# Optimization experiments

Measured on AMD Instinct MI355X. Metric: run time of the kernel, lower is better.

## Reference

```python
import jax, jax.numpy as jnp
import numpy as np

TOP_K = 2  # matches init_kwargs top_k


def setup_inputs() -> dict:
    key = jax.random.key(0)
    ks = jax.random.split(key, 7)
    d_model, d_ff, E = 512, 2048, 8
    B, S = 2, 2048
    std = 0.02
    return {
        "x": jax.random.normal(ks[0], (B, S, d_model), dtype=jnp.float32),
        "Wr": jax.random.normal(ks[1], (E, d_model), dtype=jnp.float32) * std,
        "br": jnp.zeros((E,), dtype=jnp.float32),
        "W1": jax.random.normal(ks[2], (E, d_model, d_ff), dtype=jnp.float32) * (1.0 / np.sqrt(d_model)),
        "b1": jnp.zeros((E, d_ff), dtype=jnp.float32),
        "W2": jax.random.normal(ks[3], (E, d_ff, d_model), dtype=jnp.float32) * (1.0 / np.sqrt(d_ff)),
        "b2": jnp.zeros((E, d_model), dtype=jnp.float32),
    }


def _moe_forward(x, Wr, br, W1, b1, W2, b2):
    leading = x.shape[:-1]
    d = x.shape[-1]
    E = Wr.shape[0]
    xf = x.reshape(-1, d)                                   # [N, d]
    N = xf.shape[0]

    # --- token router (linear head) ---
    logits = xf @ Wr.T + br                                  # [N, E]
    routing = jax.nn.softmax(logits, axis=-1)                # [N, E]
    sel_w, sel_idx = jax.lax.top_k(routing, TOP_K)           # [N, K]
    sel_w = sel_w / jnp.sum(sel_w, axis=-1, keepdims=True)   # renormalize top-k

    # combine weights as dense [N, E] (zero for unselected experts)
    combine = jnp.zeros((N, E), dtype=xf.dtype).at[
        jnp.arange(N)[:, None], sel_idx
    ].add(sel_w)                                             # [N, E]

    # --- expert FFNs (dense all-expert compute, masked combine) ---
    h = jax.nn.gelu(jnp.einsum("nd,edf->enf", xf, W1) + b1[:, None, :])  # [E, N, ff]
    y = jnp.einsum("enf,efd->end", h, W2) + b2[:, None, :]               # [E, N, d]

    out = jnp.einsum("ne,end->nd", combine, y)               # [N, d]
    return out.reshape(*leading, d)


def reference(x, Wr, br, W1, b1, W2, b2):
    return _moe_forward(x, Wr, br, W1, b1, W2, b2)
```

## Files before the change

kernel.cpp:

```cpp
#include <hip/hip_runtime.h>
#include <hip/hip_bf16.h>
#include <cstdint>

typedef unsigned short u16;
typedef __bf16 bf16_t;
typedef __bf16 bf16x8 __attribute__((ext_vector_type(8)));
typedef float f32x4 __attribute__((ext_vector_type(4)));

#define DM   512
#define DFF  2048
#define NEXP 8

__device__ __forceinline__ u16 f2bf(float f) {
  bf16_t b = (bf16_t)f;
  return __builtin_bit_cast(u16, b);
}
__device__ __forceinline__ uint32_t pack_bf2(float lo, float hi) {
  return (uint32_t)f2bf(lo) | ((uint32_t)f2bf(hi) << 16);
}
__device__ __forceinline__ float gelu_tanh(float x) {
  float x3 = x * x * x;
  float z = 0.7978845608028654f * (x + 0.044715f * x3);
  float az = fabsf(z);
  float e = __expf(2.0f * az);
  float t = 1.0f - 2.0f / (e + 1.0f);
  t = copysignf(t, z);
  return 0.5f * x * (1.0f + t);
}
__device__ __forceinline__ void async16(const u16* g, u16* l) {
  __builtin_amdgcn_global_load_lds((const __attribute__((address_space(1))) void*)g,
                                   (__attribute__((address_space(3))) void*)l, 16, 0, 0);
}

__device__ __forceinline__ void transpose_tile(const float* __restrict__ s,
                                               u16* __restrict__ d, int R, int C,
                                               int tileIdx) {
  __shared__ u16 tile[64][66];
  int tilesC = C >> 6;
  int bR = (tileIdx / tilesC) << 6;
  int bC = (tileIdx % tilesC) << 6;
  int rr = threadIdx.x >> 4;
  int cc = (threadIdx.x & 15) << 2;
#pragma unroll
  for (int i = 0; i < 4; ++i) {
    int r = (i << 4) + rr;
    float4 v = *(const float4*)(s + (size_t)(bR + r) * C + bC + cc);
    *(uint32_t*)&tile[r][cc]     = pack_bf2(v.x, v.y);
    *(uint32_t*)&tile[r][cc + 2] = pack_bf2(v.z, v.w);
  }
  __syncthreads();
  int c0 = threadIdx.x >> 5;
  int j  = (threadIdx.x & 31) << 1;
#pragma unroll
  for (int i = 0; i < 8; ++i) {
    int c = (i << 3) + c0;
    uint32_t v = (uint32_t)tile[j][c] | ((uint32_t)tile[j + 1][c] << 16);
    *(uint32_t*)(&d[(size_t)(bC + c) * R + bR + j]) = v;
  }
}

__global__ void k_prep(const float* __restrict__ W1, u16* __restrict__ W1T,
                       const float* __restrict__ W2, u16* __restrict__ W2T,
                       const float* __restrict__ x, u16* __restrict__ Xb,
                       const float* __restrict__ Wr, const float* __restrict__ br,
                       int* __restrict__ sel_idx, float* __restrict__ sel_w, int Ntok) {
  int b = blockIdx.x;
  if (b < 2048) {
    int e = b >> 8, t = b & 255;
    transpose_tile(W1 + (size_t)e * DM * DFF, W1T + (size_t)e * DM * DFF, DM, DFF, t);
    return;
  }
  if (b < 4096) {
    int e = (b - 2048) >> 8, t = (b - 2048) & 255;
    transpose_tile(W2 + (size_t)e * DFF * DM, W2T + (size_t)e * DFF * DM, DFF, DM, t);
    return;
  }
  if (b < 5120) {
    size_t base = ((size_t)(b - 4096) << 11) + ((size_t)threadIdx.x << 3);
    float4 a = *(const float4*)(x + base);
    float4 c = *(const float4*)(x + base + 4);
    uint4 o;
    o.x = pack_bf2(a.x, a.y);
    o.y = pack_bf2(a.z, a.w);
    o.z = pack_bf2(c.x, c.y);
    o.w = pack_bf2(c.z, c.w);
    *(uint4*)(Xb + base) = o;
    return;
  }
  int rb = b - 5120;
  int wid = threadIdx.x >> 6;
  int lane = threadIdx.x & 63;
  int tok = (rb << 2) + wid;
  if (tok >= Ntok) return;
  const float4* xr = (const float4*)(x + (size_t)tok * DM);
  float4 x0 = xr[lane * 2], x1 = xr[lane * 2 + 1];
  float logit[NEXP];
#pragma unroll
  for (int e = 0; e < NEXP; ++e) {
    const float4* wr = (const float4*)(Wr + e * DM);
    float4 w0 = wr[lane * 2], w1 = wr[lane * 2 + 1];
    float p = x0.x * w0.x + x0.y * w0.y + x0.z * w0.z + x0.w * w0.w
            + x1.x * w1.x + x1.y * w1.y + x1.z * w1.z + x1.w * w1.w;
#pragma unroll
    for (int off = 32; off; off >>= 1) p += __shfl_xor(p, off, 64);
    logit[e] = p + br[e];
  }
  if (lane == 0) {
    float mx = logit[0];
#pragma unroll
    for (int e = 1; e < NEXP; ++e) mx = fmaxf(mx, logit[e]);
    float pr[NEXP];
#pragma unroll
    for (int e = 0; e < NEXP; ++e) pr[e] = __expf(logit[e] - mx);
    int i0 = 0;
#pragma unroll
    for (int e = 1; e < NEXP; ++e) if (pr[e] > pr[i0]) i0 = e;
    int i1 = -1;
#pragma unroll
    for (int e = 0; e < NEXP; ++e) {
      if (e == i0) continue;
      if (i1 < 0 || pr[e] > pr[i1]) i1 = e;
    }
    float s2 = pr[i0] + pr[i1];
    sel_idx[tok * 2]     = i0;
    sel_idx[tok * 2 + 1] = i1;
    sel_w[tok * 2]       = pr[i0] / s2;
    sel_w[tok * 2 + 1]   = pr[i1] / s2;
  }
}

__global__ void k_scatter(const int* __restrict__ sel_idx, const float* __restrict__ sel_w,
                          int npairs, int* __restrict__ row_token, float* __restrict__ row_w,
                          int* __restrict__ pos_of, int* __restrict__ tileMeta,
                          int* __restrict__ gMeta) {
  __shared__ int cnt[NEXP], offs[NEXP], cur[NEXP];
  int tid = threadIdx.x;
  int lane = tid & 63;
  if (tid < NEXP) { cnt[tid] = 0; cur[tid] = 0; }
  __syncthreads();
  for (int p = tid; p < npairs; p += blockDim.x) {
    int e = sel_idx[p];
#pragma unroll
    for (int ex = 0; ex < NEXP; ++ex) {
      unsigned long long m = __ballot(e == ex);
      if (lane == 0 && m) atomicAdd(&cnt[ex], __popcll(m));
    }
  }
  __syncthreads();
  if (tid == 0) {
    int o = 0, nmt = 0;
    for (int e = 0; e < NEXP; ++e) {
      offs[e] = o;
      int c = cnt[e];
      int nt = (c + 127) >> 7;
      for (int t = 0; t < nt; ++t) {
        tileMeta[nmt * 3 + 0] = o + t * 128;
        tileMeta[nmt * 3 + 1] = o + c;
        tileMeta[nmt * 3 + 2] = e;
        ++nmt;
      }
      o += c;
    }
    gMeta[0] = nmt;
  }
  __syncthreads();
  for (int p = tid; p < npairs; p += blockDim.x) {
    int e = sel_idx[p];
    int pos = 0;
#pragma unroll
    for (int ex = 0; ex < NEXP; ++ex) {
      unsigned long long m = __ballot(e == ex);
      if (m) {
        int leader = __ffsll((long long)m) - 1;
        int base = 0;
        if (lane == leader) base = atomicAdd(&cur[ex], __popcll(m));
        base = __shfl(base, leader, 64);
        if (e == ex)
          pos = offs[ex] + base + __popcll(m & ((1ull << lane) - 1ull));
      }
    }
    row_token[pos] = p >> 1;
    row_w[pos] = sel_w[p];
    pos_of[p] = pos;
  }
}

template <int NFULL, int KTOT, int KCHUNK, bool GELU, bool SCALE, bool OUTBF16, bool USEMAP>
__launch_bounds__(256)
__global__ void k_gemm(const u16* __restrict__ A, const int* __restrict__ rowMap,
                       const u16* __restrict__ BT,
                       const float* __restrict__ bias, const float* __restrict__ row_w,
                       void* __restrict__ Out, size_t pstride,
                       const int* __restrict__ tileMeta, const int* __restrict__ gMeta,
                       int maxmt) {
  constexpr int NT = NFULL / 128;
  constexpr int NK = KCHUNK / 32;
  int NB = gridDim.x;
  int bid = blockIdx.x;
  int wg = ((NB & 7) == 0) ? ((bid & 7) * (NB >> 3) + (bid >> 3)) : bid;
  int nt = wg % NT;
  int rem = wg / NT;
  int mt = rem % maxmt;
  int split = rem / maxmt;
  if (mt >= gMeta[0]) return;
  int posStart = tileMeta[mt * 3 + 0];
  int segEnd   = tileMeta[mt * 3 + 1];
  int e        = tileMeta[mt * 3 + 2];

  __shared__ __align__(16) u16 smem[24576];

  int tid = threadIdx.x, lane = tid & 63, wid = tid >> 6;
  int wm = wid >> 1, wn = wid & 1;

  const u16* Abase = A + (size_t)split * KCHUNK;
  const u16* Bbase = BT + ((size_t)e * NFULL + (size_t)nt * 128) * KTOT + (size_t)split * KCHUNK;

  int l4 = lane >> 2, c4 = lane & 3;
  const u16* aS[2];
  const u16* bS[2];
#pragma unroll
  for (int i = 0; i < 2; ++i) {
    int r = i * 64 + wid * 16 + l4;
    int gra = posStart + r;
    if (gra >= segEnd) gra = segEnd - 1;
    if constexpr (USEMAP) gra = rowMap[gra];
    int cs = c4 ^ ((r >> 1) & 3);
    aS[i] = Abase + (size_t)gra * KTOT + cs * 8;
    bS[i] = Bbase + (size_t)r * KTOT + cs * 8;
  }

  auto stage = [&](int kt, int buf) {
    u16* as = smem + buf * 8192;
    u16* bs = as + 4096;
#pragma unroll
    for (int i = 0; i < 2; ++i) {
      async16(aS[i] + kt * 32, as + i * 2048 + wid * 512);
      async16(bS[i] + kt * 32, bs + i * 2048 + wid * 512);
    }
  };

  f32x4 acc[4][4] = {};

  stage(0, 0);
  stage(1, 1);
  int bufC = 0, bufS = 2;
#pragma unroll 1
  for (int t = 0; t < NK; ++t) {
    if (t + 1 < NK) asm volatile("s_waitcnt vmcnt(4)" ::: "memory");
    else            asm volatile("s_waitcnt vmcnt(0)" ::: "memory");
    __builtin_amdgcn_s_barrier();
    asm volatile("" ::: "memory");
    if (t + 2 < NK) { stage(t + 2, bufS); bufS = (bufS == 2) ? 0 : bufS + 1; }
    const char* AsB = (const char*)(smem + bufC * 8192);
    const char* BsB = AsB + 8192;
    int kb = (lane >> 4) << 4;
    bf16x8 av[4], bv[4];
#pragma unroll
    for (int mi = 0; mi < 4; ++mi) {
      int row = (wm << 6) + (mi << 4) + (lane & 15);
      av[mi] = *(const bf16x8*)(AsB + row * 64 + (kb ^ (((row >> 1) & 3) << 4)));
    }
#pragma unroll
    for (int ni = 0; ni < 4; ++ni) {
      int row = (wn << 6) + (ni << 4) + (lane & 15);
      bv[ni] = *(const bf16x8*)(BsB + row * 64 + (kb ^ (((row >> 1) & 3) << 4)));
    }
    __builtin_amdgcn_s_setprio(1);
#pragma unroll
    for (int mi = 0; mi < 4; ++mi)
#pragma unroll
      for (int ni = 0; ni < 4; ++ni)
        acc[mi][ni] = __builtin_amdgcn_mfma_f32_16x16x32_bf16(av[mi], bv[ni], acc[mi][ni], 0, 0, 0);
    __builtin_amdgcn_s_setprio(0);
    bufC = (bufC == 2) ? 0 : bufC + 1;
  }

  int laneCol = lane & 15;
  int laneRow4 = (lane >> 4) << 2;
  const float* biasE = bias + (size_t)e * NFULL;

  if constexpr (OUTBF16) {
    __syncthreads();
    u16* Cs = smem;
#pragma unroll
    for (int mi = 0; mi < 4; ++mi) {
#pragma unroll
      for (int j = 0; j < 4; ++j) {
        int r = (wm << 6) + (mi << 4) + laneRow4 + j;
#pragma unroll
        for (int ni = 0; ni < 4; ++ni) {
          int cl = (wn << 6) + (ni << 4) + laneCol;
          float v = acc[mi][ni][j] + biasE[(nt << 7) + cl];
          if constexpr (GELU) v = gelu_tanh(v);
          Cs[r * 136 + cl] = f2bf(v);
        }
      }
    }
    __syncthreads();
    int r0 = tid >> 4, q = tid & 15;
    u16* OutU = (u16*)Out;
#pragma unroll
    for (int i = 0; i < 8; ++i) {
      int r = (i << 4) + r0;
      if (posStart + r < segEnd)
        *((uint4*)(OutU + (size_t)(posStart + r) * NFULL + (nt << 7)) + q) =
            ((uint4*)(Cs + (size_t)r * 136))[q];
    }
  } else {
    float* OutF = (float*)Out + (size_t)split * pstride;
#pragma unroll
    for (int mi = 0; mi < 4; ++mi) {
#pragma unroll
      for (int j = 0; j < 4; ++j) {
        int m = posStart + (wm << 6) + (mi << 4) + laneRow4 + j;
        if (m < segEnd) {
          float w = 1.0f;
          if constexpr (SCALE) w = row_w[m];
#pragma unroll
          for (int ni = 0; ni < 4; ++ni) {
            int n = (nt << 7) + (wn << 6) + (ni << 4) + laneCol;
            float v = acc[mi][ni][j] + (split == 0 ? biasE[n] : 0.0f);
            OutF[(size_t)m * NFULL + n] = v * w;
          }
        }
      }
    }
  }
}

__global__ void k_combine(const float* __restrict__ P, size_t pstride,
                          const int* __restrict__ pos_of, float* __restrict__ out, int Ntok) {
  int tok = (blockIdx.x << 2) + (threadIdx.x >> 6);
  int lane = threadIdx.x & 63;
  if (tok >= Ntok) return;
  int p0 = pos_of[tok * 2], p1 = pos_of[tok * 2 + 1];
  const float4* a0 = (const float4*)(P + (size_t)p0 * DM);
  const float4* a1 = (const float4*)(P + pstride + (size_t)p0 * DM);
  const float4* b0 = (const float4*)(P + (size_t)p1 * DM);
  const float4* b1 = (const float4*)(P + pstride + (size_t)p1 * DM);
  float4* o = (float4*)(out + (size_t)tok * DM);
#pragma unroll
  for (int i = 0; i < 2; ++i) {
    int idx = lane * 2 + i;
    float4 x0 = a0[idx], x1 = a1[idx], y0 = b0[idx], y1 = b1[idx];
    o[idx] = make_float4(x0.x + x1.x + y0.x + y1.x,
                         x0.y + x1.y + y0.y + y1.y,
                         x0.z + x1.z + y0.z + y1.z,
                         x0.w + x1.w + y0.w + y1.w);
  }
}

extern "C" void kernel_launch(void* const* d_in, const int* in_sizes, int n_in,
                              void* d_out, int out_size, void* d_ws, size_t ws_size,
                              hipStream_t stream) {
  const float* x  = (const float*)d_in[0];
  const float* Wr = (const float*)d_in[1];
  const float* br = (const float*)d_in[2];
  const float* W1 = (const float*)d_in[3];
  const float* b1 = (const float*)d_in[4];
  const float* W2 = (const float*)d_in[5];
  const float* b2 = (const float*)d_in[6];
  float* out = (float*)d_out;

  int Ntok = in_sizes[0] / DM;
  int npairs = Ntok * 2;
  int maxmt = npairs / 128 + NEXP;
  size_t pstride = (size_t)npairs * DM;

  char* p = (char*)d_ws;
  u16* W1T = (u16*)p;  p += (size_t)NEXP * DFF * DM * 2;
  u16* W2T = (u16*)p;  p += (size_t)NEXP * DM * DFF * 2;
  u16* Xb  = (u16*)p;  p += (size_t)Ntok * DM * 2;
  u16* H   = (u16*)p;  p += (size_t)npairs * DFF * 2;
  float* Part = (float*)p; p += 2 * pstride * 4;
  int* sel_idx   = (int*)p;   p += (size_t)npairs * 4;
  float* sel_w   = (float*)p; p += (size_t)npairs * 4;
  int* pos_of    = (int*)p;   p += (size_t)npairs * 4;
  int* row_token = (int*)p;   p += (size_t)npairs * 4;
  float* row_w   = (float*)p; p += (size_t)npairs * 4;
  int* tileMeta  = (int*)p;   p += (size_t)(maxmt * 3 + 16) * 4;
  int* gMeta     = (int*)p;   p += 64;

  k_prep<<<dim3(5120 + Ntok / 4), 256, 0, stream>>>(W1, W1T, W2, W2T, x, Xb, Wr, br,
                                                    sel_idx, sel_w, Ntok);
  k_scatter<<<dim3(1), 1024, 0, stream>>>(sel_idx, sel_w, npairs, row_token, row_w,
                                          pos_of, tileMeta, gMeta);
  k_gemm<DFF, DM, DM, true, false, true, true>
      <<<dim3(maxmt * (DFF / 128)), 256, 0, stream>>>(
          Xb, row_token, W1T, b1, nullptr, H, 0, tileMeta, gMeta, maxmt);
  k_gemm<DM, DFF, DFF / 2, false, true, false, false>
      <<<dim3(maxmt * (DM / 128) * 2), 256, 0, stream>>>(
          H, nullptr, W2T, b2, row_w, Part, pstride, tileMeta, gMeta, maxmt);
  k_combine<<<dim3(Ntok / 4), 256, 0, stream>>>(Part, pstride, pos_of, out, Ntok);
}
```

Baseline: 140.3 us.

## Widen transpose stores, parallelize scatter per expert, store split-K partials in bf16

The weight transpose now writes 16-byte vectors instead of 4-byte words. The routing scatter runs one block per expert instead of a single block. The second GEMM writes its split-K partial outputs as bf16 through the shared-memory staged path, and the combine kernel reads bf16. This halves the partial-buffer traffic and cuts scatter serialization, at the cost of extra rounding error in the partial sums.

```diff
diff --git a/kernel.cpp b/kernel.cpp
--- a/kernel.cpp
+++ b/kernel.cpp
@@ -49,13 +49,16 @@
     *(uint32_t*)&tile[r][cc + 2] = pack_bf2(v.z, v.w);
   }
   __syncthreads();
-  int c0 = threadIdx.x >> 5;
-  int j  = (threadIdx.x & 31) << 1;
-#pragma unroll
-  for (int i = 0; i < 8; ++i) {
-    int c = (i << 3) + c0;
-    uint32_t v = (uint32_t)tile[j][c] | ((uint32_t)tile[j + 1][c] << 16);
-    *(uint32_t*)(&d[(size_t)(bC + c) * R + bR + j]) = v;
+  int c  = threadIdx.x >> 3;
+  int j0 = (threadIdx.x & 7) << 3;
+#pragma unroll
+  for (int half = 0; half < 2; ++half) {
+    int cc2 = c + (half << 5);
+    uint32_t w0 = (uint32_t)tile[j0 + 0][cc2] | ((uint32_t)tile[j0 + 1][cc2] << 16);
+    uint32_t w1 = (uint32_t)tile[j0 + 2][cc2] | ((uint32_t)tile[j0 + 3][cc2] << 16);
+    uint32_t w2 = (uint32_t)tile[j0 + 4][cc2] | ((uint32_t)tile[j0 + 5][cc2] << 16);
+    uint32_t w3 = (uint32_t)tile[j0 + 6][cc2] | ((uint32_t)tile[j0 + 7][cc2] << 16);
+    *(uint4*)(&d[(size_t)(bC + cc2) * R + bR + j0]) = make_uint4(w0, w1, w2, w3);
   }
 }
 
@@ -133,10 +136,12 @@
                           int npairs, int* __restrict__ row_token, float* __restrict__ row_w,
                           int* __restrict__ pos_of, int* __restrict__ tileMeta,
                           int* __restrict__ gMeta) {
-  __shared__ int cnt[NEXP], offs[NEXP], cur[NEXP];
+  __shared__ int cnt[NEXP], offs[NEXP], cur;
+  int eb = blockIdx.x;
   int tid = threadIdx.x;
   int lane = tid & 63;
-  if (tid < NEXP) { cnt[tid] = 0; cur[tid] = 0; }
+  if (tid < NEXP) cnt[tid] = 0;
+  if (tid == 0) cur = 0;
   __syncthreads();
   for (int p = tid; p < npairs; p += blockDim.x) {
     int e = sel_idx[p];
@@ -148,40 +153,39 @@
   }
   __syncthreads();
   if (tid == 0) {
-    int o = 0, nmt = 0;
-    for (int e = 0; e < NEXP; ++e) {
-      offs[e] = o;
-      int c = cnt[e];
-      int nt = (c + 127) >> 7;
-      for (int t = 0; t < nt; ++t) {
-        tileMeta[nmt * 3 + 0] = o + t * 128;
-        tileMeta[nmt * 3 + 1] = o + c;
-        tileMeta[nmt * 3 + 2] = e;
-        ++nmt;
+    int o = 0;
+    for (int e = 0; e < NEXP; ++e) { offs[e] = o; o += cnt[e]; }
+    if (eb == 0) {
+      int nmt = 0;
+      for (int e = 0; e < NEXP; ++e) {
+        int c = cnt[e];
+        int nt = (c + 127) >> 7;
+        for (int t = 0; t < nt; ++t) {
+          tileMeta[nmt * 3 + 0] = offs[e] + t * 128;
+          tileMeta[nmt * 3 + 1] = offs[e] + c;
+          tileMeta[nmt * 3 + 2] = e;
+          ++nmt;
+        }
       }
-      o += c;
-    }
-    gMeta[0] = nmt;
+      gMeta[0] = nmt;
+    }
   }
   __syncthreads();
   for (int p = tid; p < npairs; p += blockDim.x) {
     int e = sel_idx[p];
-    int pos = 0;
-#pragma unroll
-    for (int ex = 0; ex < NEXP; ++ex) {
-      unsigned long long m = __ballot(e == ex);
-      if (m) {
-        int leader = __ffsll((long long)m) - 1;
-        int base = 0;
-        if (lane == leader) base = atomicAdd(&cur[ex], __popcll(m));
-        base = __shfl(base, leader, 64);
-        if (e == ex)
-          pos = offs[ex] + base + __popcll(m & ((1ull << lane) - 1ull));
+    unsigned long long m = __ballot(e == eb);
+    if (m) {
+      int leader = __ffsll((long long)m) - 1;
+      int base = 0;
+      if (lane == leader) base = atomicAdd(&cur, __popcll(m));
+      base = __shfl(base, leader, 64);
+      if (e == eb) {
+        int pos = offs[eb] + base + __popcll(m & ((1ull << lane) - 1ull));
+        row_token[pos] = p >> 1;
+        row_w[pos] = sel_w[p];
+        pos_of[p] = pos;
       }
     }
-    row_token[pos] = p >> 1;
-    row_w[pos] = sel_w[p];
-    pos_of[p] = pos;
   }
 }
 
@@ -287,18 +291,23 @@
 #pragma unroll
       for (int j = 0; j < 4; ++j) {
         int r = (wm << 6) + (mi << 4) + laneRow4 + j;
+        int m = posStart + r;
+        int mc = m < segEnd ? m : segEnd - 1;
+        float w = 1.0f;
+        if constexpr (SCALE) w = row_w[mc];
 #pragma unroll
         for (int ni = 0; ni < 4; ++ni) {
           int cl = (wn << 6) + (ni << 4) + laneCol;
-          float v = acc[mi][ni][j] + biasE[(nt << 7) + cl];
+          float v = acc[mi][ni][j] + (split == 0 ? biasE[(nt << 7) + cl] : 0.0f);
           if constexpr (GELU) v = gelu_tanh(v);
+          if constexpr (SCALE) v *= w;
           Cs[r * 136 + cl] = f2bf(v);
         }
       }
     }
     __syncthreads();
     int r0 = tid >> 4, q = tid & 15;
-    u16* OutU = (u16*)Out;
+    u16* OutU = (u16*)Out + (size_t)split * pstride;
 #pragma unroll
     for (int i = 0; i < 8; ++i) {
       int r = (i << 4) + r0;
@@ -328,26 +337,24 @@
   }
 }
 
-__global__ void k_combine(const float* __restrict__ P, size_t pstride,
+template <int NSPLIT>
+__global__ void k_combine(const u16* __restrict__ P, size_t pstride,
                           const int* __restrict__ pos_of, float* __restrict__ out, int Ntok) {
   int tok = (blockIdx.x << 2) + (threadIdx.x >> 6);
   int lane = threadIdx.x & 63;
   if (tok >= Ntok) return;
   int p0 = pos_of[tok * 2], p1 = pos_of[tok * 2 + 1];
-  const float4* a0 = (const float4*)(P + (size_t)p0 * DM);
-  const float4* a1 = (const float4*)(P + pstride + (size_t)p0 * DM);
-  const float4* b0 = (const float4*)(P + (size_t)p1 * DM);
-  const float4* b1 = (const float4*)(P + pstride + (size_t)p1 * DM);
-  float4* o = (float4*)(out + (size_t)tok * DM);
-#pragma unroll
-  for (int i = 0; i < 2; ++i) {
-    int idx = lane * 2 + i;
-    float4 x0 = a0[idx], x1 = a1[idx], y0 = b0[idx], y1 = b1[idx];
-    o[idx] = make_float4(x0.x + x1.x + y0.x + y1.x,
-                         x0.y + x1.y + y0.y + y1.y,
-                         x0.z + x1.z + y0.z + y1.z,
-                         x0.w + x1.w + y0.w + y1.w);
-  }
+  float s[8] = {};
+#pragma unroll
+  for (int sp = 0; sp < NSPLIT; ++sp) {
+    bf16x8 a = ((const bf16x8*)(P + sp * pstride + (size_t)p0 * DM))[lane];
+    bf16x8 b = ((const bf16x8*)(P + sp * pstride + (size_t)p1 * DM))[lane];
+#pragma unroll
+    for (int i = 0; i < 8; ++i) s[i] += (float)a[i] + (float)b[i];
+  }
+  float4* o = (float4*)(out + (size_t)tok * DM + lane * 8);
+  o[0] = make_float4(s[0], s[1], s[2], s[3]);
+  o[1] = make_float4(s[4], s[5], s[6], s[7]);
 }
 
 extern "C" void kernel_launch(void* const* d_in, const int* in_sizes, int n_in,
@@ -372,7 +379,7 @@
   u16* W2T = (u16*)p;  p += (size_t)NEXP * DM * DFF * 2;
   u16* Xb  = (u16*)p;  p += (size_t)Ntok * DM * 2;
   u16* H   = (u16*)p;  p += (size_t)npairs * DFF * 2;
-  float* Part = (float*)p; p += 2 * pstride * 4;
+  u16* Part = (u16*)p; p += 2 * pstride * 2;
   int* sel_idx   = (int*)p;   p += (size_t)npairs * 4;
   float* sel_w   = (float*)p; p += (size_t)npairs * 4;
   int* pos_of    = (int*)p;   p += (size_t)npairs * 4;
@@ -383,13 +390,13 @@
 
   k_prep<<<dim3(5120 + Ntok / 4), 256, 0, stream>>>(W1, W1T, W2, W2T, x, Xb, Wr, br,
                                                     sel_idx, sel_w, Ntok);
-  k_scatter<<<dim3(1), 1024, 0, stream>>>(sel_idx, sel_w, npairs, row_token, row_w,
-                                          pos_of, tileMeta, gMeta);
+  k_scatter<<<dim3(NEXP), 1024, 0, stream>>>(sel_idx, sel_w, npairs, row_token, row_w,
+                                             pos_of, tileMeta, gMeta);
   k_gemm<DFF, DM, DM, true, false, true, true>
       <<<dim3(maxmt * (DFF / 128)), 256, 0, stream>>>(
           Xb, row_token, W1T, b1, nullptr, H, 0, tileMeta, gMeta, maxmt);
-  k_gemm<DM, DFF, DFF / 2, false, true, false, false>
+  k_gemm<DM, DFF, DFF / 2, false, true, true, false>
       <<<dim3(maxmt * (DM / 128) * 2), 256, 0, stream>>>(
           H, nullptr, W2T, b2, row_w, Part, pstride, tileMeta, gMeta, maxmt);
-  k_combine<<<dim3(Ntok / 4), 256, 0, stream>>>(Part, pstride, pos_of, out, Ntok);
-}
+  k_combine<2><<<dim3(Ntok / 4), 256, 0, stream>>>(Part, pstride, pos_of, out, Ntok);
+}
```

Result: faster. 132.7 us (-5.4%).
